# Optimization experiments

Measured on AMD Instinct MI355X. Metric: run time of the kernel, lower is better.

Reference implementation:

```python
import jax, jax.numpy as jnp
import numpy as np

H = 4  # num_heads
EPS = 1e-5


def setup_inputs() -> dict:
    key = jax.random.key(0)
    ks = jax.random.split(key, 12)
    N, C, E = 4096, 128, 131072
    x = jax.random.normal(ks[0], (N, C), dtype=jnp.float32)
    edge_index = jax.random.randint(ks[1], (2, E), 0, N, dtype=jnp.int64)
    # guarantee every row has at least one neighbor (self-loops) to avoid NaN softmax rows
    loops = jnp.arange(N, dtype=jnp.int64)
    edge_index = edge_index.at[0, :N].set(loops).at[1, :N].set(loops)
    s = 1.0 / np.sqrt(C)
    def lin(k):
        kw, kb = jax.random.split(k)
        return (jax.random.uniform(kw, (C, C), jnp.float32, -s, s),
                jax.random.uniform(kb, (C,), jnp.float32, -s, s))
    wq, bq = lin(ks[2]); wk, bk = lin(ks[3]); wv, bv = lin(ks[4]); wo, bo = lin(ks[5])
    gamma = jnp.ones((C,), jnp.float32)
    beta = jnp.zeros((C,), jnp.float32)
    return {"x": x, "edge_index": edge_index, "wq": wq, "bq": bq, "wk": wk, "bk": bk,
            "wv": wv, "bv": bv, "wo": wo, "bo": bo, "gamma": gamma, "beta": beta}


def reference(x, edge_index, wq, bq, wk, bk, wv, bv, wo, bo, gamma, beta):
    N, C = x.shape
    D = C // H
    q = (x @ wq.T + bq).reshape(N, H, D)
    k = (x @ wk.T + bk).reshape(N, H, D)
    v = (x @ wv.T + bv).reshape(N, H, D)
    scores = jnp.einsum('nhd,mhd->nhm', q, k) / jnp.sqrt(jnp.float32(D))  # [N,H,N]
    row, col = edge_index
    mask = jnp.zeros((N, N), jnp.float32).at[row, col].set(1.0)
    scores = jnp.where(mask[:, None, :] == 0, -jnp.inf, scores)
    attn = jax.nn.softmax(scores, axis=-1)  # dropout is identity in eval
    out = jnp.einsum('nhm,mhd->nhd', attn, v).reshape(N, C)
    out = out @ wo.T + bo
    y = x + out
    mu = jnp.mean(y, axis=-1, keepdims=True)
    var = jnp.var(y, axis=-1, keepdims=True)
    return (y - mu) / jnp.sqrt(var + EPS) * gamma + beta
```

## Files before the change

### kernel.cpp

```cpp
#include <hip/hip_runtime.h>

typedef unsigned long long u64;

#define C_DIM 128
#define MAXN 128

__global__ __launch_bounds__(256) void prep_kernel(
    u64* __restrict__ bm, int bm_words,
    const float* __restrict__ wq, const float* __restrict__ wk,
    const float* __restrict__ wv, const float* __restrict__ wo,
    float* __restrict__ wqT, float* __restrict__ wkT,
    float* __restrict__ wvT, float* __restrict__ woT)
{
    int tid = blockIdx.x * 256 + threadIdx.x;
    int stride = gridDim.x * 256;
    for (int i = tid; i < bm_words; i += stride) bm[i] = 0ull;
    const float* Ws[4] = {wq, wk, wv, wo};
    float*       Ts[4] = {wqT, wkT, wvT, woT};
    for (int idx = tid; idx < 4 * C_DIM * C_DIM; idx += stride) {
        int m = idx >> 14;
        int e = idx & 16383;
        int j = e >> 7, c = e & 127;
        Ts[m][c * C_DIM + j] = Ws[m][e];
    }
}

__global__ __launch_bounds__(256, 4) void build_qkv_kernel(
    const int* __restrict__ ei, int E, u64* __restrict__ bm, int wpr,
    const float* __restrict__ x,
    const float* __restrict__ wqT, const float* __restrict__ bq,
    const float* __restrict__ wkT, const float* __restrict__ bk,
    const float* __restrict__ wvT, const float* __restrict__ bv,
    float* __restrict__ qo, float* __restrict__ ko, float* __restrict__ vo)
{
    const int ROWS = 8;
    __shared__ float xs[ROWS][C_DIM];
    int t = threadIdx.x;
    int n0 = blockIdx.x * ROWS;
    int stride = gridDim.x * 256;
    for (int e = blockIdx.x * 256 + t; e < E; e += stride) {
        int r = ei[e], c = ei[E + e];
        atomicOr(&bm[(size_t)r * wpr + (c >> 6)], 1ull << (c & 63));
    }
    {
        int r = t >> 5, c4 = (t & 31) << 2;
        *(float4*)&xs[r][c4] = *(const float4*)(x + (size_t)(n0 + r) * C_DIM + c4);
    }
    __syncthreads();
    int j4 = (t & 31) << 2;
    int r  = t >> 5;
    float4 aq = *(const float4*)(bq + j4);
    float4 ak = *(const float4*)(bk + j4);
    float4 av = *(const float4*)(bv + j4);
    #pragma unroll 2
    for (int c = 0; c < C_DIM; c += 4) {
        #pragma unroll
        for (int u = 0; u < 4; ++u) {
            float4 q4 = *(const float4*)(wqT + (size_t)(c + u) * C_DIM + j4);
            float4 k4 = *(const float4*)(wkT + (size_t)(c + u) * C_DIM + j4);
            float4 v4 = *(const float4*)(wvT + (size_t)(c + u) * C_DIM + j4);
            float xv = xs[r][c + u];
            aq.x += xv * q4.x; aq.y += xv * q4.y; aq.z += xv * q4.z; aq.w += xv * q4.w;
            ak.x += xv * k4.x; ak.y += xv * k4.y; ak.z += xv * k4.z; ak.w += xv * k4.w;
            av.x += xv * v4.x; av.y += xv * v4.y; av.z += xv * v4.z; av.w += xv * v4.w;
        }
    }
    size_t o = (size_t)(n0 + r) * C_DIM + j4;
    *(float4*)(qo + o) = aq;
    *(float4*)(ko + o) = ak;
    *(float4*)(vo + o) = av;
}

__global__ __launch_bounds__(256, 4) void attn_oln_kernel(
    const float* __restrict__ q, const float* __restrict__ k,
    const float* __restrict__ v, const u64* __restrict__ bm, int wpr,
    const float* __restrict__ x,
    const float* __restrict__ woT, const float* __restrict__ bo,
    const float* __restrict__ gamma, const float* __restrict__ beta,
    float* __restrict__ out)
{
    const int ROWS = 4;
    __shared__ float qs[ROWS][C_DIM];
    __shared__ float xs[ROWS][C_DIM];
    __shared__ int   lm[ROWS][MAXN];
    __shared__ float ls[ROWS][4][MAXN];
    int t = threadIdx.x;
    int n0 = blockIdx.x * ROWS;
    int wave = t >> 6, lane = t & 63;
    const float scale = 0.17677669529663687f;

    int n = n0 + wave;
    qs[wave][lane]      = q[(size_t)n * C_DIM + lane] * scale;
    qs[wave][64 + lane] = q[(size_t)n * C_DIM + 64 + lane] * scale;
    u64 bits = bm[(size_t)n * wpr + lane];
    int pc = __popcll(bits);
    int incl = pc;
    #pragma unroll
    for (int off = 1; off < 64; off <<= 1) {
        int tv = __shfl_up(incl, off);
        if (lane >= off) incl += tv;
    }
    int cnt = __shfl(incl, 63);
    int pos = incl - pc;
    u64 bb = bits;
    while (bb) {
        int b = __builtin_ctzll(bb);
        bb &= bb - 1;
        if (pos < MAXN) lm[wave][pos] = (lane << 6) + b;
        ++pos;
    }
    if (cnt > MAXN) cnt = MAXN;
    __syncthreads();
    {
        int nb = lane & 15, hh = lane >> 4;
        float4 qf[8];
        #pragma unroll
        for (int u = 0; u < 8; ++u)
            qf[u] = *(const float4*)&qs[wave][hh * 32 + u * 4];
        for (int j0 = 0; j0 < cnt; j0 += 16) {
            int jj = j0 + nb;
            if (jj < cnt) {
                const float* kr = k + (size_t)lm[wave][jj] * C_DIM + hh * 32;
                float s = 0.f;
                #pragma unroll
                for (int u = 0; u < 8; ++u) {
                    float4 k4 = *(const float4*)(kr + u * 4);
                    s += qf[u].x * k4.x + qf[u].y * k4.y
                       + qf[u].z * k4.z + qf[u].w * k4.w;
                }
                ls[wave][hh][jj] = s;
            }
        }
    }
    __syncthreads();
    int g = lane >> 4, li = lane & 15;
    float mx = -1e30f;
    for (int jj = li; jj < cnt; jj += 16) mx = fmaxf(mx, ls[wave][g][jj]);
    #pragma unroll
    for (int off = 8; off; off >>= 1) mx = fmaxf(mx, __shfl_xor(mx, off));
    float sum = 0.f;
    for (int jj = li; jj < cnt; jj += 16) {
        float e = __expf(ls[wave][g][jj] - mx);
        ls[wave][g][jj] = e;
        sum += e;
    }
    #pragma unroll
    for (int off = 8; off; off >>= 1) sum += __shfl_xor(sum, off);
    float sinv = 1.0f / sum;
    __syncthreads();
    int h0 = lane >> 5;
    float s0 = __shfl(sinv, h0 * 16);
    float s1 = __shfl(sinv, (h0 + 2) * 16);
    float a0 = 0.f, a1 = 0.f;
    for (int j0 = 0; j0 < cnt; j0 += 8) {
        int cc = cnt - j0; if (cc > 8) cc = 8;
        float v0a[8], v1a[8], w0a[8], w1a[8];
        #pragma unroll
        for (int u = 0; u < 8; ++u) {
            if (u < cc) {
                int m = lm[wave][j0 + u];
                v0a[u] = v[(size_t)m * C_DIM + lane];
                v1a[u] = v[(size_t)m * C_DIM + 64 + lane];
                w0a[u] = ls[wave][h0][j0 + u];
                w1a[u] = ls[wave][h0 + 2][j0 + u];
            }
        }
        #pragma unroll
        for (int u = 0; u < 8; ++u) {
            if (u < cc) { a0 += w0a[u] * v0a[u]; a1 += w1a[u] * v1a[u]; }
        }
    }
    xs[wave][lane]      = a0 * s0;
    xs[wave][64 + lane] = a1 * s1;
    __syncthreads();
    int r  = t >> 6;
    int j2 = (t & 63) << 1;
    float2 acc = *(const float2*)(bo + j2);
    #pragma unroll 2
    for (int c = 0; c < C_DIM; c += 4) {
        #pragma unroll
        for (int u = 0; u < 4; ++u) {
            float2 w2 = *(const float2*)(woT + (size_t)(c + u) * C_DIM + j2);
            float xv = xs[r][c + u];
            acc.x += xv * w2.x;
            acc.y += xv * w2.y;
        }
    }
    __syncthreads();
    {
        float2 xr = *(const float2*)(x + (size_t)(n0 + r) * C_DIM + j2);
        xs[r][j2]     = acc.x + xr.x;
        xs[r][j2 + 1] = acc.y + xr.y;
    }
    __syncthreads();
    {
        float y0 = xs[wave][lane], y1 = xs[wave][64 + lane];
        float s = y0 + y1, s2 = y0 * y0 + y1 * y1;
        #pragma unroll
        for (int off = 32; off; off >>= 1) {
            s  += __shfl_xor(s, off);
            s2 += __shfl_xor(s2, off);
        }
        float mu = s * (1.0f / 128.0f);
        float var = s2 * (1.0f / 128.0f) - mu * mu;
        float rstd = rsqrtf(var + 1e-5f);
        size_t o = (size_t)n * C_DIM;
        out[o + lane]      = (y0 - mu) * rstd * gamma[lane] + beta[lane];
        out[o + 64 + lane] = (y1 - mu) * rstd * gamma[64 + lane] + beta[64 + lane];
    }
}

extern "C" void kernel_launch(void* const* d_in, const int* in_sizes, int n_in,
                              void* d_out, int out_size, void* d_ws, size_t ws_size,
                              hipStream_t stream)
{
    const float* x     = (const float*)d_in[0];
    const int*   ei    = (const int*)d_in[1];
    const float* wq    = (const float*)d_in[2];
    const float* bq    = (const float*)d_in[3];
    const float* wk    = (const float*)d_in[4];
    const float* bk    = (const float*)d_in[5];
    const float* wv    = (const float*)d_in[6];
    const float* bv    = (const float*)d_in[7];
    const float* wo    = (const float*)d_in[8];
    const float* bo    = (const float*)d_in[9];
    const float* gamma = (const float*)d_in[10];
    const float* beta  = (const float*)d_in[11];
    float* out = (float*)d_out;

    int N = in_sizes[0] / C_DIM;
    int E = in_sizes[1] / 2;
    int wpr = N >> 6;

    size_t mat_bytes = (size_t)N * C_DIM * sizeof(float);
    size_t wT_bytes  = (size_t)C_DIM * C_DIM * sizeof(float);
    char* base = (char*)d_ws;
    float* q   = (float*)(base);
    float* k   = (float*)(base + mat_bytes);
    float* v   = (float*)(base + 2 * mat_bytes);
    u64*   bm  = (u64*)(base + 3 * mat_bytes);
    float* wqT = (float*)(base + 4 * mat_bytes);
    float* wkT = (float*)(base + 4 * mat_bytes + wT_bytes);
    float* wvT = (float*)(base + 4 * mat_bytes + 2 * wT_bytes);
    float* woT = (float*)(base + 4 * mat_bytes + 3 * wT_bytes);

    int bm_words = N * wpr;
    prep_kernel<<<64, 256, 0, stream>>>(bm, bm_words, wq, wk, wv, wo,
                                        wqT, wkT, wvT, woT);
    build_qkv_kernel<<<N / 8, 256, 0, stream>>>(ei, E, bm, wpr,
                                                x, wqT, bq, wkT, bk, wvT, bv, q, k, v);
    attn_oln_kernel<<<N / 4, 256, 0, stream>>>(q, k, v, bm, wpr,
                                               x, woT, bo, gamma, beta, out);
}
```

Measured before the change: 139.9 us.

## Memset the bitmap, coalesce transposes, widen QKV blocks, unroll gather deeper

The adjacency bitmap is now zeroed with hipMemsetAsync instead of inside the prep kernel. The weight transpose is changed to do coalesced writes with strided reads. build_qkv_kernel moves to 512 threads per block, each computing two output columns instead of four, and handles one edge per thread without a grid-stride loop. That edge handling assumes the grid covers E. The attention value-gather loop is unrolled to 16 neighbors, and softmax weights are read straight from LDS instead of being staged in registers.

```diff
diff --git a/kernel.cpp b/kernel.cpp
--- a/kernel.cpp
+++ b/kernel.cpp
@@ -6,7 +6,6 @@
 #define MAXN 128
 
 __global__ __launch_bounds__(256) void prep_kernel(
-    u64* __restrict__ bm, int bm_words,
     const float* __restrict__ wq, const float* __restrict__ wk,
     const float* __restrict__ wv, const float* __restrict__ wo,
     float* __restrict__ wqT, float* __restrict__ wkT,
@@ -14,18 +13,17 @@
 {
     int tid = blockIdx.x * 256 + threadIdx.x;
     int stride = gridDim.x * 256;
-    for (int i = tid; i < bm_words; i += stride) bm[i] = 0ull;
     const float* Ws[4] = {wq, wk, wv, wo};
     float*       Ts[4] = {wqT, wkT, wvT, woT};
     for (int idx = tid; idx < 4 * C_DIM * C_DIM; idx += stride) {
         int m = idx >> 14;
         int e = idx & 16383;
-        int j = e >> 7, c = e & 127;
-        Ts[m][c * C_DIM + j] = Ws[m][e];
-    }
-}
-
-__global__ __launch_bounds__(256, 4) void build_qkv_kernel(
+        int c = e >> 7, j = e & 127;
+        Ts[m][e] = Ws[m][j * C_DIM + c];
+    }
+}
+
+__global__ __launch_bounds__(512, 4) void build_qkv_kernel(
     const int* __restrict__ ei, int E, u64* __restrict__ bm, int wpr,
     const float* __restrict__ x,
     const float* __restrict__ wqT, const float* __restrict__ bq,
@@ -37,38 +35,40 @@
     __shared__ float xs[ROWS][C_DIM];
     int t = threadIdx.x;
     int n0 = blockIdx.x * ROWS;
-    int stride = gridDim.x * 256;
-    for (int e = blockIdx.x * 256 + t; e < E; e += stride) {
-        int r = ei[e], c = ei[E + e];
-        atomicOr(&bm[(size_t)r * wpr + (c >> 6)], 1ull << (c & 63));
-    }
-    {
+    {
+        int e = blockIdx.x * 512 + t;
+        if (e < E) {
+            int r = ei[e], c = ei[E + e];
+            atomicOr(&bm[(size_t)r * wpr + (c >> 6)], 1ull << (c & 63));
+        }
+    }
+    if (t < 256) {
         int r = t >> 5, c4 = (t & 31) << 2;
         *(float4*)&xs[r][c4] = *(const float4*)(x + (size_t)(n0 + r) * C_DIM + c4);
     }
     __syncthreads();
-    int j4 = (t & 31) << 2;
-    int r  = t >> 5;
-    float4 aq = *(const float4*)(bq + j4);
-    float4 ak = *(const float4*)(bk + j4);
-    float4 av = *(const float4*)(bv + j4);
+    int j2 = (t & 63) << 1;
+    int r  = t >> 6;
+    float2 aq = *(const float2*)(bq + j2);
+    float2 ak = *(const float2*)(bk + j2);
+    float2 av = *(const float2*)(bv + j2);
     #pragma unroll 2
     for (int c = 0; c < C_DIM; c += 4) {
         #pragma unroll
         for (int u = 0; u < 4; ++u) {
-            float4 q4 = *(const float4*)(wqT + (size_t)(c + u) * C_DIM + j4);
-            float4 k4 = *(const float4*)(wkT + (size_t)(c + u) * C_DIM + j4);
-            float4 v4 = *(const float4*)(wvT + (size_t)(c + u) * C_DIM + j4);
+            float2 q2 = *(const float2*)(wqT + (size_t)(c + u) * C_DIM + j2);
+            float2 k2 = *(const float2*)(wkT + (size_t)(c + u) * C_DIM + j2);
+            float2 v2 = *(const float2*)(wvT + (size_t)(c + u) * C_DIM + j2);
             float xv = xs[r][c + u];
-            aq.x += xv * q4.x; aq.y += xv * q4.y; aq.z += xv * q4.z; aq.w += xv * q4.w;
-            ak.x += xv * k4.x; ak.y += xv * k4.y; ak.z += xv * k4.z; ak.w += xv * k4.w;
-            av.x += xv * v4.x; av.y += xv * v4.y; av.z += xv * v4.z; av.w += xv * v4.w;
-        }
-    }
-    size_t o = (size_t)(n0 + r) * C_DIM + j4;
-    *(float4*)(qo + o) = aq;
-    *(float4*)(ko + o) = ak;
-    *(float4*)(vo + o) = av;
+            aq.x += xv * q2.x; aq.y += xv * q2.y;
+            ak.x += xv * k2.x; ak.y += xv * k2.y;
+            av.x += xv * v2.x; av.y += xv * v2.y;
+        }
+    }
+    size_t o = (size_t)(n0 + r) * C_DIM + j2;
+    *(float2*)(qo + o) = aq;
+    *(float2*)(ko + o) = ak;
+    *(float2*)(vo + o) = av;
 }
 
 __global__ __launch_bounds__(256, 4) void attn_oln_kernel(
@@ -152,22 +152,23 @@
     float s0 = __shfl(sinv, h0 * 16);
     float s1 = __shfl(sinv, (h0 + 2) * 16);
     float a0 = 0.f, a1 = 0.f;
-    for (int j0 = 0; j0 < cnt; j0 += 8) {
-        int cc = cnt - j0; if (cc > 8) cc = 8;
-        float v0a[8], v1a[8], w0a[8], w1a[8];
-        #pragma unroll
-        for (int u = 0; u < 8; ++u) {
+    for (int j0 = 0; j0 < cnt; j0 += 16) {
+        int cc = cnt - j0; if (cc > 16) cc = 16;
+        float v0a[16], v1a[16];
+        #pragma unroll
+        for (int u = 0; u < 16; ++u) {
             if (u < cc) {
                 int m = lm[wave][j0 + u];
                 v0a[u] = v[(size_t)m * C_DIM + lane];
                 v1a[u] = v[(size_t)m * C_DIM + 64 + lane];
-                w0a[u] = ls[wave][h0][j0 + u];
-                w1a[u] = ls[wave][h0 + 2][j0 + u];
             }
         }
         #pragma unroll
-        for (int u = 0; u < 8; ++u) {
-            if (u < cc) { a0 += w0a[u] * v0a[u]; a1 += w1a[u] * v1a[u]; }
+        for (int u = 0; u < 16; ++u) {
+            if (u < cc) {
+                a0 += ls[wave][h0][j0 + u] * v0a[u];
+                a1 += ls[wave][h0 + 2][j0 + u] * v1a[u];
+            }
         }
     }
     xs[wave][lane]      = a0 * s0;
@@ -244,10 +245,9 @@
     float* wvT = (float*)(base + 4 * mat_bytes + 2 * wT_bytes);
     float* woT = (float*)(base + 4 * mat_bytes + 3 * wT_bytes);
 
-    int bm_words = N * wpr;
-    prep_kernel<<<64, 256, 0, stream>>>(bm, bm_words, wq, wk, wv, wo,
-                                        wqT, wkT, wvT, woT);
-    build_qkv_kernel<<<N / 8, 256, 0, stream>>>(ei, E, bm, wpr,
+    hipMemsetAsync(bm, 0, (size_t)N * wpr * sizeof(u64), stream);
+    prep_kernel<<<32, 256, 0, stream>>>(wq, wk, wv, wo, wqT, wkT, wvT, woT);
+    build_qkv_kernel<<<N / 8, 512, 0, stream>>>(ei, E, bm, wpr,
                                                 x, wqT, bq, wkT, bk, wvT, bv, q, k, v);
     attn_oln_kernel<<<N / 4, 256, 0, stream>>>(q, k, v, bm, wpr,
                                                x, woT, bo, gamma, beta, out);
```

After: 163.6 us. 1.17x slower.
